# Kernel optimization log

Measured on AMD Instinct MI355X. Metric: run time of the kernel, lower is better.

The kernel has to match this reference:

```python
import jax, jax.numpy as jnp
import numpy as np

N_QUBITS = 12
N_LAYERS = 2
INPUT_DIM = 8
HIDDEN_DIM = 4
SEQ_LEN = 16
BATCH = 64


def _apply_1q(state, gate, wire):
    # state: (B,) + (2,)*n complex64; gate: (2,2) or (B,2,2)
    s = jnp.moveaxis(state, wire + 1, 1)
    sh = s.shape
    s = s.reshape(sh[0], 2, -1)
    if gate.ndim == 2:
        s = jnp.einsum('ij,bjk->bik', gate, s)
    else:
        s = jnp.einsum('bij,bjk->bik', gate, s)
    return jnp.moveaxis(s.reshape(sh), 1, wire + 1)


def _apply_cnot(state, c, t):
    s = jnp.moveaxis(state, (c + 1, t + 1), (1, 2))  # (B,2,2,rest)
    s = jnp.concatenate([s[:, :1], s[:, 1:, ::-1]], axis=1)  # flip target where control=1
    return jnp.moveaxis(s, (1, 2), (c + 1, t + 1))


def _rx_gates(angles):
    # per-sample RX(theta) = [[cos(t/2), -i sin(t/2)], [-i sin(t/2), cos(t/2)]]
    c = jnp.cos(angles / 2).astype(jnp.complex64)
    s = (-1j) * jnp.sin(angles / 2).astype(jnp.complex64)
    return jnp.stack([jnp.stack([c, s], -1), jnp.stack([s, c], -1)], -2)  # (B,2,2)


def _rot_gate(phi, theta, omega):
    # PennyLane Rot(phi,theta,omega) = RZ(omega) RY(theta) RZ(phi)
    c = jnp.cos(theta / 2).astype(jnp.complex64)
    s = jnp.sin(theta / 2).astype(jnp.complex64)
    m00 = jnp.exp(-0.5j * (phi + omega)) * c
    m01 = -jnp.exp(0.5j * (phi - omega)) * s
    m10 = jnp.exp(-0.5j * (phi - omega)) * s
    m11 = jnp.exp(0.5j * (phi + omega)) * c
    return jnp.stack([jnp.stack([m00, m01]), jnp.stack([m10, m11])])


def _circuit(angles, weights):
    # angles: (B, n_qubits); weights: (L, n_qubits, 3) -> (B, n_qubits) PauliZ expvals
    n = N_QUBITS
    B = angles.shape[0]
    state = jnp.zeros((B,) + (2,) * n, jnp.complex64)
    state = state.at[(slice(None),) + (0,) * n].set(1.0)
    for i in range(angles.shape[1]):
        state = _apply_1q(state, _rx_gates(angles[:, i]), i)
    for l in range(N_LAYERS):
        for i in range(n):
            state = _apply_1q(state, _rot_gate(weights[l, i, 0], weights[l, i, 1], weights[l, i, 2]), i)
        r = l % (n - 1) + 1  # StronglyEntanglingLayers default ranges
        for i in range(n):
            state = _apply_cnot(state, i, (i + r) % n)
    p = state.real ** 2 + state.imag ** 2
    z = []
    for i in range(n):
        q = jnp.moveaxis(p, i + 1, 1).reshape(B, 2, -1).sum(-1)
        z.append(q[:, 0] - q[:, 1])
    return jnp.stack(z, axis=1)


def setup_inputs() -> dict:
    key = jax.random.key(0)
    ks = jax.random.split(key, 16)
    inp = {
        'inputs': jax.random.normal(ks[0], (SEQ_LEN, BATCH, INPUT_DIM), jnp.float32),
        'forget_weights': jax.random.normal(ks[1], (N_LAYERS, N_QUBITS, 3), jnp.float32),
        'input_weights': jax.random.normal(ks[2], (N_LAYERS, N_QUBITS, 3), jnp.float32),
        'update_weights': jax.random.normal(ks[3], (N_LAYERS, N_QUBITS, 3), jnp.float32),
        'output_weights': jax.random.normal(ks[4], (N_LAYERS, N_QUBITS, 3), jnp.float32),
        'fW': jax.random.normal(ks[5], (HIDDEN_DIM, N_QUBITS), jnp.float32) * 0.3,
        'fb': jax.random.normal(ks[6], (HIDDEN_DIM,), jnp.float32) * 0.1,
        'iW': jax.random.normal(ks[7], (HIDDEN_DIM, N_QUBITS), jnp.float32) * 0.3,
        'ib': jax.random.normal(ks[8], (HIDDEN_DIM,), jnp.float32) * 0.1,
        'uW': jax.random.normal(ks[9], (HIDDEN_DIM, N_QUBITS), jnp.float32) * 0.3,
        'ub': jax.random.normal(ks[10], (HIDDEN_DIM,), jnp.float32) * 0.1,
        'oW': jax.random.normal(ks[11], (HIDDEN_DIM, N_QUBITS), jnp.float32) * 0.3,
        'ob': jax.random.normal(ks[12], (HIDDEN_DIM,), jnp.float32) * 0.1,
    }
    return inp


def reference(inputs, forget_weights, input_weights, update_weights, output_weights,
              fW, fb, iW, ib, uW, ub, oW, ob):
    S, B, D = inputs.shape
    H = fb.shape[0]
    h0 = jnp.zeros((B, H), inputs.dtype)
    c0 = jnp.zeros((B, H), inputs.dtype)

    def step(carry, x):
        hx, cx = carry
        comb = jnp.concatenate([x, hx], axis=1)  # (B, n_qubits)
        f = jax.nn.sigmoid(_circuit(comb, forget_weights) @ fW.T + fb)
        i = jax.nn.sigmoid(_circuit(comb, input_weights) @ iW.T + ib)
        g = jnp.tanh(_circuit(comb, update_weights) @ uW.T + ub)
        o = jax.nn.sigmoid(_circuit(comb, output_weights) @ oW.T + ob)
        cx = f * cx + i * g
        hx = o * jnp.tanh(cx)
        return (hx, cx), hx

    (hx, cx), outputs = jax.lax.scan(jax.checkpoint(step), (h0, c0), inputs)
    return outputs, hx, cx
```

## Files before the change

### kernel.cpp

```cpp
#include <hip/hip_runtime.h>
#include <math.h>

#define AGENT __HIP_MEMORY_SCOPE_AGENT


__device__ __forceinline__ float ftanh(float x) {
    x = fminf(fmaxf(x, -15.f), 15.f);
    const float e = __expf(2.f * x);
    return (e - 1.f) / (e + 1.f);
}
__device__ __forceinline__ float fsigm(float x) { return 1.f / (1.f + __expf(-x)); }
__device__ __forceinline__ float gld(const float* p) {
    return __hip_atomic_load(p, __ATOMIC_RELAXED, AGENT);
}

#define CMUL(dr, di, xr, xi, yr, yi) \
    do { dr = (xr)*(yr) - (xi)*(yi); di = (xr)*(yi) + (xi)*(yr); } while (0)

template<int CTRL>
__device__ __forceinline__ float dppf(float x) {
    return __int_as_float(__builtin_amdgcn_update_dpp(
        0, __float_as_int(x), CTRL, 0xF, 0xF, true));
}

template<int CTRL>
__device__ __forceinline__ void dpprot(float ar[8], float ai[8],
                                       float por, float poi, float ppr, float ppi) {
#pragma unroll
    for (int j = 0; j < 8; ++j) {
        const float qr = dppf<CTRL>(ar[j]);
        const float qi = dppf<CTRL>(ai[j]);
        const float nr = por*ar[j] - poi*ai[j] + ppr*qr - ppi*qi;
        const float ni = por*ai[j] + poi*ar[j] + ppr*qi + ppi*qr;
        ar[j] = nr; ai[j] = ni;
    }
}

__device__ __forceinline__ void shflrot32(float ar[8], float ai[8],
                                          float por, float poi, float ppr, float ppi) {
#pragma unroll
    for (int j = 0; j < 8; ++j) {
        const float qr = __shfl_xor(ar[j], 32);
        const float qi = __shfl_xor(ai[j], 32);
        const float nr = por*ar[j] - poi*ai[j] + ppr*qr - ppi*qi;
        const float ni = por*ai[j] + poi*ar[j] + ppr*qi + ppi*qr;
        ar[j] = nr; ai[j] = ni;
    }
}

__device__ __forceinline__ void rot3(float ar[8], float ai[8],
                                     const float* __restrict__ g3) {
    float gm[24];
#pragma unroll
    for (int k = 0; k < 6; ++k) ((float4*)gm)[k] = ((const float4*)g3)[k];
#pragma unroll
    for (int k = 0; k < 3; ++k) {
        const float m0=gm[k*8+0], m1=gm[k*8+1], m2=gm[k*8+2], m3=gm[k*8+3];
        const float m4=gm[k*8+4], m5=gm[k*8+5], m6=gm[k*8+6], m7=gm[k*8+7];
        const int vs = 4 >> k;
#pragma unroll
        for (int p = 0; p < 4; ++p) {
            const int lowm = vs - 1;
            const int j0 = ((p & ~lowm) << 1) | (p & lowm);
            const int j1 = j0 | vs;
            const float a0r = ar[j0], a0i = ai[j0];
            const float a1r = ar[j1], a1i = ai[j1];
            ar[j0] = m0*a0r - m1*a0i + m2*a1r - m3*a1i;
            ai[j0] = m0*a0i + m1*a0r + m2*a1i + m3*a1r;
            ar[j1] = m4*a0r - m5*a0i + m6*a1r - m7*a1i;
            ai[j1] = m4*a0i + m5*a0r + m6*a1i + m7*a1r;
        }
    }
}

__global__ __launch_bounds__(512, 2)
void qlstm_fused(const float* __restrict__ inputs,
                 const float* __restrict__ wf, const float* __restrict__ wi,
                 const float* __restrict__ wu, const float* __restrict__ wo,
                 const float* __restrict__ fW, const float* __restrict__ fb,
                 const float* __restrict__ iW, const float* __restrict__ ib,
                 const float* __restrict__ uW, const float* __restrict__ ub,
                 const float* __restrict__ oW, const float* __restrict__ ob,
                 float* __restrict__ gact,
                 unsigned* __restrict__ ctr,
                 float* __restrict__ out)
{
    __shared__ float2 bufA[4096], bufB[4096];
    __shared__ __align__(16) float rotm[192];
    __shared__ __align__(16) float4 wtab[12];
    __shared__ float Wsh[48];
    __shared__ float zred[8][4];

    const int tid = threadIdx.x;
    const int b = blockIdx.x & 63;
    const int g = blockIdx.x >> 6;
    const int l = tid & 63, w = tid >> 6;

    const float* wsel = (g == 0) ? wf : (g == 1) ? wi : (g == 2) ? wu : wo;
    const float* Wsel = (g == 0) ? fW : (g == 1) ? iW : (g == 2) ? uW : oW;
    const float* bsel = (g == 0) ? fb : (g == 1) ? ib : (g == 2) ? ub : ob;

    if (tid < 24) {
        const int k = tid;
        const float phi = wsel[k*3+0], th = wsel[k*3+1], om = wsel[k*3+2];
        float ct, sth; __sincosf(0.5f * th, &sth, &ct);
        float ca, sa;  __sincosf(0.5f * (phi + om), &sa, &ca);
        float cb, sb2; __sincosf(0.5f * (phi - om), &sb2, &cb);
        float* m = rotm + k * 8;
        m[0] =  ca * ct;  m[1] = -sa * ct;
        m[2] = -cb * sth; m[3] = -sb2 * sth;
        m[4] =  cb * sth; m[5] = -sb2 * sth;
        m[6] =  ca * ct;  m[7] =  sa * ct;
    }
    if (tid < 48) Wsh[tid] = Wsel[tid];
    const float bu = (tid < 4) ? bsel[tid] : 0.f;
    __syncthreads();

    const int MSK[12] = {0x555,0xAAA,0x554,0xAA8,0x550,0xAA0,
                         0x540,0xA80,0x500,0xA00,0x155,0x2AA};
    const int qbase = ((l >> 5) << 8) | (w << 5) | (((l >> 3) & 3) << 3) | (l & 7);
    float4 Qv[8];
#pragma unroll
    for (int s = 0; s < 8; ++s) {
        float q0 = 0.f, q1 = 0.f, q2 = 0.f, q3 = 0.f;
        const int idx = qbase | (s << 9);
#pragma unroll
        for (int p = 0; p < 12; ++p) {
            const float sgn = (__popc(idx & MSK[p]) & 1) ? -1.f : 1.f;
            const int m = 11 - p;
            q0 += sgn * Wsh[m];
            q1 += sgn * Wsh[12 + m];
            q2 += sgn * Wsh[24 + m];
            q3 += sgn * Wsh[36 + m];
        }
        Qv[s] = make_float4(q0, q1, q2, q3);
    }

    const int X0 = (tid << 3) ^ (tid << 2);
    int bitq[7];
#pragma unroll
    for (int qq = 0; qq < 7; ++qq) bitq[qq] = (X0 >> (9 - qq)) & 1;
    const int b11 = (tid >> 8) & 1;
    const int b10 = ((tid >> 7) & 1) ^ b11;
    const int lx  = tid & 1;
    const int wbase = (tid << 3) ^ (tid & 15);
    const int rb1 = ((w << 9) | (((l >> 5) & 1) << 8) |
                     (((l >> 3) & 3) << 3) | (l & 7)) ^ ((l >> 3) & 3);
    const int rb2 = ((l << 3) | w) ^ (l & 15);
    const int be8 = l & 1, be7 = (l >> 1) & 1, be3 = (l >> 5) & 1;

    float c_ = 0.f, h_ = 0.f;

    for (int t = 0; t < 16; ++t) {
        if (tid >= 64 && tid < 72) {
            const int q = tid - 64;
            float sn, cs; __sincosf(0.5f * inputs[t*512 + b*8 + q], &sn, &cs);
            const float* m = rotm + q * 8;
            wtab[q] = make_float4(m[0]*cs + m[3]*sn, m[1]*cs - m[2]*sn,
                                  m[4]*cs + m[7]*sn, m[5]*cs - m[6]*sn);
        }
        if (tid < 4) {
            if (t > 0) {
                while (__hip_atomic_load(&ctr[b*16 + (t-1)],
                                         __ATOMIC_RELAXED, AGENT) < 4u)
                    __builtin_amdgcn_s_sleep(2);
                __threadfence();
                const float* ga = gact + ((t-1)&1)*1024 + b*4 + tid;
                const float f_ = gld(ga),       i_ = gld(ga + 256);
                const float u_ = gld(ga + 512), o_ = gld(ga + 768);
                c_ = f_*c_ + i_*u_;
                h_ = o_*ftanh(c_);
                if (g == 0) out[(t-1)*256 + b*4 + tid] = h_;
            }
            float sn, cs; __sincosf(0.5f * h_, &sn, &cs);
            const float* m = rotm + (8 + tid) * 8;
            wtab[8 + tid] = make_float4(m[0]*cs + m[3]*sn, m[1]*cs - m[2]*sn,
                                        m[4]*cs + m[7]*sn, m[5]*cs - m[6]*sn);
        }
        __syncthreads();

        const float* wf4 = (const float*)wtab;
        float Pr, Pi;
        {
            const float2 f0 = *(const float2*)(wf4 + 2*4 + bitq[0]*2);
            Pr = f0.x; Pi = f0.y;
#pragma unroll
            for (int qq = 1; qq < 7; ++qq) {
                const float2 f = *(const float2*)(wf4 + (2+qq)*4 + bitq[qq]*2);
                float nr, ni; CMUL(nr, ni, Pr, Pi, f.x, f.y);
                Pr = nr; Pi = ni;
            }
        }
        const float4 R0 = wtab[0], R1 = wtab[1];
        const float4 R9 = wtab[9], RA = wtab[10], RB = wtab[11];
        const float v0sr = b11 ? R0.z : R0.x, v0si = b11 ? R0.w : R0.y;
        const float v0or = b11 ? R0.x : R0.z, v0oi = b11 ? R0.y : R0.w;
        const float v1sr = b10 ? R1.z : R1.x, v1si = b10 ? R1.w : R1.y;
        const float v1or = b10 ? R1.x : R1.z, v1oi = b10 ? R1.y : R1.w;
        float Er, Ei, Og, Oh;
        CMUL(Er, Ei, v0sr, v0si, v1sr, v1si);
        CMUL(Og, Oh, v0or, v0oi, v1or, v1oi);
        float PEr, PEi, POr, POi;
        CMUL(PEr, PEi, Pr, Pi, Er, Ei);
        CMUL(POr, POi, Pr, Pi, Og, Oh);
        const float w9lr = lx ? R9.z : R9.x, w9li = lx ? R9.w : R9.y;
        const float w9hr = lx ? R9.x : R9.z, w9hi = lx ? R9.y : R9.w;
        float m0r,m0i, m1r,m1i, m2r,m2i, m3r,m3i;
        CMUL(m0r,m0i, w9lr,w9li, RA.x,RA.y);
        CMUL(m1r,m1i, w9lr,w9li, RA.z,RA.w);
        CMUL(m2r,m2i, w9hr,w9hi, RA.x,RA.y);
        CMUL(m3r,m3i, w9hr,w9hi, RA.z,RA.w);
        float ttr[8], tti[8];
        CMUL(ttr[0],tti[0], m0r,m0i, RB.x,RB.y);
        CMUL(ttr[1],tti[1], m0r,m0i, RB.z,RB.w);
        CMUL(ttr[2],tti[2], m1r,m1i, RB.x,RB.y);
        CMUL(ttr[3],tti[3], m1r,m1i, RB.z,RB.w);
        CMUL(ttr[4],tti[4], m2r,m2i, RB.x,RB.y);
        CMUL(ttr[5],tti[5], m2r,m2i, RB.z,RB.w);
        CMUL(ttr[6],tti[6], m3r,m3i, RB.x,RB.y);
        CMUL(ttr[7],tti[7], m3r,m3i, RB.z,RB.w);
        float ar[8], ai[8];
        CMUL(ar[0],ai[0], PEr,PEi, ttr[0],tti[0]);
        CMUL(ar[1],ai[1], POr,POi, ttr[1],tti[1]);
        CMUL(ar[2],ai[2], PEr,PEi, ttr[3],tti[3]);
        CMUL(ar[3],ai[3], POr,POi, ttr[2],tti[2]);
        CMUL(ar[4],ai[4], PEr,PEi, ttr[6],tti[6]);
        CMUL(ar[5],ai[5], POr,POi, ttr[7],tti[7]);
        CMUL(ar[6],ai[6], PEr,PEi, ttr[5],tti[5]);
        CMUL(ar[7],ai[7], POr,POi, ttr[4],tti[4]);

        rot3(ar, ai, rotm + 168);
        {
            const float4 row = *(const float4*)(rotm + 160 + (be8 << 2));
            const float por = be8 ? row.z : row.x, poi = be8 ? row.w : row.y;
            const float ppr = be8 ? row.x : row.z, ppi = be8 ? row.y : row.w;
            dpprot<0xB1>(ar, ai, por, poi, ppr, ppi);
        }
        {
            const float4 row = *(const float4*)(rotm + 152 + (be7 << 2));
            const float por = be7 ? row.z : row.x, poi = be7 ? row.w : row.y;
            const float ppr = be7 ? row.x : row.z, ppi = be7 ? row.y : row.w;
            dpprot<0x4E>(ar, ai, por, poi, ppr, ppi);
        }
        {
            const float4 row = *(const float4*)(rotm + 120 + (be3 << 2));
            const float por = be3 ? row.z : row.x, poi = be3 ? row.w : row.y;
            const float ppr = be3 ? row.x : row.z, ppi = be3 ? row.y : row.w;
            shflrot32(ar, ai, por, poi, ppr, ppi);
        }
#pragma unroll
        for (int s = 0; s < 8; ++s)
            bufA[wbase ^ s] = make_float2(ar[s], ai[s]);
        __syncthreads();
#pragma unroll
        for (int s = 0; s < 8; ++s) {
            const float2 v = bufA[(rb1 | (s << 5)) ^ ((s & 3) << 2)];
            ar[s] = v.x; ai[s] = v.y;
        }
        rot3(ar, ai, rotm + 128);
#pragma unroll
        for (int s = 0; s < 8; ++s)
            bufB[wbase ^ s] = make_float2(ar[s], ai[s]);
        __syncthreads();
#pragma unroll
        for (int s = 0; s < 8; ++s) {
            const float2 v = bufB[rb2 | (s << 9)];
            ar[s] = v.x; ai[s] = v.y;
        }
        rot3(ar, ai, rotm + 96);

        float a0 = 0.f, a1 = 0.f, a2 = 0.f, a3 = 0.f;
#pragma unroll
        for (int s = 0; s < 8; ++s) {
            const float p = ar[s]*ar[s] + ai[s]*ai[s];
            a0 += p * Qv[s].x; a1 += p * Qv[s].y;
            a2 += p * Qv[s].z; a3 += p * Qv[s].w;
        }
#pragma unroll
        for (int off = 32; off > 0; off >>= 1) {
            a0 += __shfl_down(a0, off);
            a1 += __shfl_down(a1, off);
            a2 += __shfl_down(a2, off);
            a3 += __shfl_down(a3, off);
        }
        if (l == 0) {
            zred[w][0] = a0; zred[w][1] = a1; zred[w][2] = a2; zred[w][3] = a3;
        }
        __syncthreads();
        if (tid < 4) {
            float tot = bu;
#pragma unroll
            for (int wv = 0; wv < 8; ++wv) tot += zred[wv][tid];
            const float act = (g == 2) ? ftanh(tot) : fsigm(tot);
            __hip_atomic_store(&gact[(t&1)*1024 + g*256 + b*4 + tid], act,
                               __ATOMIC_RELAXED, AGENT);
        }
        if (tid == 0)
            __hip_atomic_fetch_add(&ctr[b*16 + t], 1u, __ATOMIC_RELEASE, AGENT);
    }

    if (g == 0 && tid < 4) {
        while (__hip_atomic_load(&ctr[b*16 + 15], __ATOMIC_RELAXED, AGENT) < 4u)
            __builtin_amdgcn_s_sleep(2);
        __threadfence();
        const float* ga = gact + 1024 + b*4 + tid;
        const float f_ = gld(ga),       i_ = gld(ga + 256);
        const float u_ = gld(ga + 512), o_ = gld(ga + 768);
        const float cn = f_*c_ + i_*u_;
        const float hn = o_*ftanh(cn);
        out[3840 + b*4 + tid] = hn;
        out[4096 + b*4 + tid] = hn;
        out[4352 + b*4 + tid] = cn;
    }
}

extern "C" void kernel_launch(void* const* d_in, const int* in_sizes, int n_in,
                              void* d_out, int out_size, void* d_ws, size_t ws_size,
                              hipStream_t stream) {
    (void)in_sizes; (void)n_in; (void)out_size; (void)ws_size;
    const float* inputs = (const float*)d_in[0];
    const float* wf = (const float*)d_in[1];
    const float* wi = (const float*)d_in[2];
    const float* wu = (const float*)d_in[3];
    const float* wo = (const float*)d_in[4];
    const float* fW = (const float*)d_in[5];
    const float* fb = (const float*)d_in[6];
    const float* iW = (const float*)d_in[7];
    const float* ib = (const float*)d_in[8];
    const float* uW = (const float*)d_in[9];
    const float* ub = (const float*)d_in[10];
    const float* oW = (const float*)d_in[11];
    const float* ob = (const float*)d_in[12];
    float* out = (float*)d_out;
    unsigned* ctr = (unsigned*)d_ws;
    float* gact = (float*)d_ws + 1024;

    hipMemsetAsync(ctr, 0, 1024 * sizeof(unsigned), stream);

    void* args[] = { (void*)&inputs, (void*)&wf, (void*)&wi, (void*)&wu, (void*)&wo,
                     (void*)&fW, (void*)&fb, (void*)&iW, (void*)&ib,
                     (void*)&uW, (void*)&ub, (void*)&oW, (void*)&ob,
                     (void*)&gact, (void*)&ctr, (void*)&out };
    hipError_t err = hipLaunchCooperativeKernel((const void*)qlstm_fused,
                                                dim3(256), dim3(512),
                                                args, 0, stream);
    if (err != hipSuccess) {
        qlstm_fused<<<dim3(256), dim3(512), 0, stream>>>(
            inputs, wf, wi, wu, wo, fW, fb, iW, ib, uW, ub, oW, ob,
            gact, ctr, out);
    }
}
```

Before: 168.2 us.

## Prefetch input-angle gates, hoist rotation matrices to registers, cheaper reduction

Double-buffers the input-encoding gate table so step t+1's sincos is computed during step t. The input-only product of the first nine qubit factors is now computed before the cross-block spin-wait and barrier, leaving only the hidden-state-dependent part on the critical path. The rotation matrices and per-lane DPP/shuffle coefficients are loaded once into registers instead of being reloaded from LDS every step. The four-value wave reduction is also replaced by a butterfly that folds the accumulators into one lane-distributed value, cutting shuffle count. The cost is higher register pressure from 72+ extra live floats, which risks spills under the 512x2 launch bound.

Measured after the change: 204.0 us (median of 3 runs). +21.3%, slower.

```diff
diff --git a/kernel.cpp b/kernel.cpp
--- a/kernel.cpp
+++ b/kernel.cpp
@@ -48,11 +48,8 @@
     }
 }
 
-__device__ __forceinline__ void rot3(float ar[8], float ai[8],
-                                     const float* __restrict__ g3) {
-    float gm[24];
-#pragma unroll
-    for (int k = 0; k < 6; ++k) ((float4*)gm)[k] = ((const float4*)g3)[k];
+__device__ __forceinline__ void rot3r(float ar[8], float ai[8],
+                                      const float* gm) {
 #pragma unroll
     for (int k = 0; k < 3; ++k) {
         const float m0=gm[k*8+0], m1=gm[k*8+1], m2=gm[k*8+2], m3=gm[k*8+3];
@@ -87,7 +84,8 @@
 {
     __shared__ float2 bufA[4096], bufB[4096];
     __shared__ __align__(16) float rotm[192];
-    __shared__ __align__(16) float4 wtab[12];
+    __shared__ __align__(16) float4 wtabx[2][8];
+    __shared__ __align__(16) float4 wtabh[4];
     __shared__ float Wsh[48];
     __shared__ float zred[8][4];
 
@@ -116,6 +114,32 @@
     const float bu = (tid < 4) ? bsel[tid] : 0.f;
     __syncthreads();
 
+    if (tid >= 64 && tid < 72) {
+        const int q = tid - 64;
+        float sn, cs; __sincosf(0.5f * inputs[b*8 + q], &sn, &cs);
+        const float* m = rotm + q * 8;
+        wtabx[0][q] = make_float4(m[0]*cs + m[3]*sn, m[1]*cs - m[2]*sn,
+                                  m[4]*cs + m[7]*sn, m[5]*cs - m[6]*sn);
+    }
+
+    const int be8 = l & 1, be7 = (l >> 1) & 1, be3 = (l >> 5) & 1;
+    float rT[24], rM[24], rL[24];
+#pragma unroll
+    for (int k = 0; k < 6; ++k) {
+        ((float4*)rT)[k] = ((const float4*)(rotm + 168))[k];
+        ((float4*)rM)[k] = ((const float4*)(rotm + 128))[k];
+        ((float4*)rL)[k] = ((const float4*)(rotm +  96))[k];
+    }
+    const float4 r8v = *(const float4*)(rotm + 160 + (be8 << 2));
+    const float por8 = be8 ? r8v.z : r8v.x, poi8 = be8 ? r8v.w : r8v.y;
+    const float ppr8 = be8 ? r8v.x : r8v.z, ppi8 = be8 ? r8v.y : r8v.w;
+    const float4 r7v = *(const float4*)(rotm + 152 + (be7 << 2));
+    const float por7 = be7 ? r7v.z : r7v.x, poi7 = be7 ? r7v.w : r7v.y;
+    const float ppr7 = be7 ? r7v.x : r7v.z, ppi7 = be7 ? r7v.y : r7v.w;
+    const float4 r3v = *(const float4*)(rotm + 120 + (be3 << 2));
+    const float por3 = be3 ? r3v.z : r3v.x, poi3 = be3 ? r3v.w : r3v.y;
+    const float ppr3 = be3 ? r3v.x : r3v.z, ppi3 = be3 ? r3v.y : r3v.w;
+
     const int MSK[12] = {0x555,0xAAA,0x554,0xAA8,0x550,0xAA0,
                          0x540,0xA80,0x500,0xA00,0x155,0x2AA};
     const int qbase = ((l >> 5) << 8) | (w << 5) | (((l >> 3) & 3) << 3) | (l & 7);
@@ -147,18 +171,45 @@
     const int rb1 = ((w << 9) | (((l >> 5) & 1) << 8) |
                      (((l >> 3) & 3) << 3) | (l & 7)) ^ ((l >> 3) & 3);
     const int rb2 = ((l << 3) | w) ^ (l & 15);
-    const int be8 = l & 1, be7 = (l >> 1) & 1, be3 = (l >> 5) & 1;
 
     float c_ = 0.f, h_ = 0.f;
 
+    __syncthreads();
+
     for (int t = 0; t < 16; ++t) {
-        if (tid >= 64 && tid < 72) {
+        const int cur = t & 1;
+        if (t < 15 && tid >= 64 && tid < 72) {
             const int q = tid - 64;
-            float sn, cs; __sincosf(0.5f * inputs[t*512 + b*8 + q], &sn, &cs);
+            float sn, cs; __sincosf(0.5f * inputs[(t+1)*512 + b*8 + q], &sn, &cs);
             const float* m = rotm + q * 8;
-            wtab[q] = make_float4(m[0]*cs + m[3]*sn, m[1]*cs - m[2]*sn,
-                                  m[4]*cs + m[7]*sn, m[5]*cs - m[6]*sn);
-        }
+            wtabx[cur ^ 1][q] = make_float4(m[0]*cs + m[3]*sn, m[1]*cs - m[2]*sn,
+                                            m[4]*cs + m[7]*sn, m[5]*cs - m[6]*sn);
+        }
+
+        const float* wx = (const float*)&wtabx[cur][0];
+        const float2 f2 = *(const float2*)(wx +  8 + bitq[0]*2);
+        const float2 f3 = *(const float2*)(wx + 12 + bitq[1]*2);
+        const float2 f4 = *(const float2*)(wx + 16 + bitq[2]*2);
+        const float2 f5 = *(const float2*)(wx + 20 + bitq[3]*2);
+        const float2 f6 = *(const float2*)(wx + 24 + bitq[4]*2);
+        const float2 f7 = *(const float2*)(wx + 28 + bitq[5]*2);
+        float a23r,a23i, a45r,a45i, a67r,a67i, p47r,p47i, P6r,P6i;
+        CMUL(a23r,a23i, f2.x,f2.y, f3.x,f3.y);
+        CMUL(a45r,a45i, f4.x,f4.y, f5.x,f5.y);
+        CMUL(a67r,a67i, f6.x,f6.y, f7.x,f7.y);
+        CMUL(p47r,p47i, a45r,a45i, a67r,a67i);
+        CMUL(P6r,P6i,   a23r,a23i, p47r,p47i);
+        const float4 R0 = wtabx[cur][0], R1 = wtabx[cur][1];
+        const float v0sr = b11 ? R0.z : R0.x, v0si = b11 ? R0.w : R0.y;
+        const float v0or = b11 ? R0.x : R0.z, v0oi = b11 ? R0.y : R0.w;
+        const float v1sr = b10 ? R1.z : R1.x, v1si = b10 ? R1.w : R1.y;
+        const float v1or = b10 ? R1.x : R1.z, v1oi = b10 ? R1.y : R1.w;
+        float Er,Ei, Og,Oh, PEr,PEi, POr,POi;
+        CMUL(Er,Ei, v0sr,v0si, v1sr,v1si);
+        CMUL(Og,Oh, v0or,v0oi, v1or,v1oi);
+        CMUL(PEr,PEi, P6r,P6i, Er,Ei);
+        CMUL(POr,POi, P6r,P6i, Og,Oh);
+
         if (tid < 4) {
             if (t > 0) {
                 while (__hip_atomic_load(&ctr[b*16 + (t-1)],
@@ -174,35 +225,16 @@
             }
             float sn, cs; __sincosf(0.5f * h_, &sn, &cs);
             const float* m = rotm + (8 + tid) * 8;
-            wtab[8 + tid] = make_float4(m[0]*cs + m[3]*sn, m[1]*cs - m[2]*sn,
-                                        m[4]*cs + m[7]*sn, m[5]*cs - m[6]*sn);
+            wtabh[tid] = make_float4(m[0]*cs + m[3]*sn, m[1]*cs - m[2]*sn,
+                                     m[4]*cs + m[7]*sn, m[5]*cs - m[6]*sn);
         }
         __syncthreads();
 
-        const float* wf4 = (const float*)wtab;
-        float Pr, Pi;
-        {
-            const float2 f0 = *(const float2*)(wf4 + 2*4 + bitq[0]*2);
-            Pr = f0.x; Pi = f0.y;
-#pragma unroll
-            for (int qq = 1; qq < 7; ++qq) {
-                const float2 f = *(const float2*)(wf4 + (2+qq)*4 + bitq[qq]*2);
-                float nr, ni; CMUL(nr, ni, Pr, Pi, f.x, f.y);
-                Pr = nr; Pi = ni;
-            }
-        }
-        const float4 R0 = wtab[0], R1 = wtab[1];
-        const float4 R9 = wtab[9], RA = wtab[10], RB = wtab[11];
-        const float v0sr = b11 ? R0.z : R0.x, v0si = b11 ? R0.w : R0.y;
-        const float v0or = b11 ? R0.x : R0.z, v0oi = b11 ? R0.y : R0.w;
-        const float v1sr = b10 ? R1.z : R1.x, v1si = b10 ? R1.w : R1.y;
-        const float v1or = b10 ? R1.x : R1.z, v1oi = b10 ? R1.y : R1.w;
-        float Er, Ei, Og, Oh;
-        CMUL(Er, Ei, v0sr, v0si, v1sr, v1si);
-        CMUL(Og, Oh, v0or, v0oi, v1or, v1oi);
-        float PEr, PEi, POr, POi;
-        CMUL(PEr, PEi, Pr, Pi, Er, Ei);
-        CMUL(POr, POi, Pr, Pi, Og, Oh);
+        const float4 W8 = wtabh[0], R9 = wtabh[1], RA = wtabh[2], RB = wtabh[3];
+        const float w8r = bitq[6] ? W8.z : W8.x, w8i = bitq[6] ? W8.w : W8.y;
+        float FEr,FEi, FOr,FOi;
+        CMUL(FEr,FEi, PEr,PEi, w8r,w8i);
+        CMUL(FOr,FOi, POr,POi, w8r,w8i);
         const float w9lr = lx ? R9.z : R9.x, w9li = lx ? R9.w : R9.y;
         const float w9hr = lx ? R9.x : R9.z, w9hi = lx ? R9.y : R9.w;
         float m0r,m0i, m1r,m1i, m2r,m2i, m3r,m3i;
@@ -220,34 +252,20 @@
         CMUL(ttr[6],tti[6], m3r,m3i, RB.x,RB.y);
         CMUL(ttr[7],tti[7], m3r,m3i, RB.z,RB.w);
         float ar[8], ai[8];
-        CMUL(ar[0],ai[0], PEr,PEi, ttr[0],tti[0]);
-        CMUL(ar[1],ai[1], POr,POi, ttr[1],tti[1]);
-        CMUL(ar[2],ai[2], PEr,PEi, ttr[3],tti[3]);
-        CMUL(ar[3],ai[3], POr,POi, ttr[2],tti[2]);
-        CMUL(ar[4],ai[4], PEr,PEi, ttr[6],tti[6]);
-        CMUL(ar[5],ai[5], POr,POi, ttr[7],tti[7]);
-        CMUL(ar[6],ai[6], PEr,PEi, ttr[5],tti[5]);
-        CMUL(ar[7],ai[7], POr,POi, ttr[4],tti[4]);
-
-        rot3(ar, ai, rotm + 168);
-        {
-            const float4 row = *(const float4*)(rotm + 160 + (be8 << 2));
-            const float por = be8 ? row.z : row.x, poi = be8 ? row.w : row.y;
-            const float ppr = be8 ? row.x : row.z, ppi = be8 ? row.y : row.w;
-            dpprot<0xB1>(ar, ai, por, poi, ppr, ppi);
-        }
-        {
-            const float4 row = *(const float4*)(rotm + 152 + (be7 << 2));
-            const float por = be7 ? row.z : row.x, poi = be7 ? row.w : row.y;
-            const float ppr = be7 ? row.x : row.z, ppi = be7 ? row.y : row.w;
-            dpprot<0x4E>(ar, ai, por, poi, ppr, ppi);
-        }
-        {
-            const float4 row = *(const float4*)(rotm + 120 + (be3 << 2));
-            const float por = be3 ? row.z : row.x, poi = be3 ? row.w : row.y;
-            const float ppr = be3 ? row.x : row.z, ppi = be3 ? row.y : row.w;
-            shflrot32(ar, ai, por, poi, ppr, ppi);
-        }
+        CMUL(ar[0],ai[0], FEr,FEi, ttr[0],tti[0]);
+        CMUL(ar[1],ai[1], FOr,FOi, ttr[1],tti[1]);
+        CMUL(ar[2],ai[2], FEr,FEi, ttr[3],tti[3]);
+        CMUL(ar[3],ai[3], FOr,FOi, ttr[2],tti[2]);
+        CMUL(ar[4],ai[4], FEr,FEi, ttr[6],tti[6]);
+        CMUL(ar[5],ai[5], FOr,FOi, ttr[7],tti[7]);
+        CMUL(ar[6],ai[6], FEr,FEi, ttr[5],tti[5]);
+        CMUL(ar[7],ai[7], FOr,FOi, ttr[4],tti[4]);
+
+        rot3r(ar, ai, rT);
+        dpprot<0xB1>(ar, ai, por8, poi8, ppr8, ppi8);
+        dpprot<0x4E>(ar, ai, por7, poi7, ppr7, ppi7);
+        shflrot32(ar, ai, por3, poi3, ppr3, ppi3);
+
 #pragma unroll
         for (int s = 0; s < 8; ++s)
             bufA[wbase ^ s] = make_float2(ar[s], ai[s]);
@@ -257,7 +275,7 @@
             const float2 v = bufA[(rb1 | (s << 5)) ^ ((s & 3) << 2)];
             ar[s] = v.x; ai[s] = v.y;
         }
-        rot3(ar, ai, rotm + 128);
+        rot3r(ar, ai, rM);
 #pragma unroll
         for (int s = 0; s < 8; ++s)
             bufB[wbase ^ s] = make_float2(ar[s], ai[s]);
@@ -267,7 +285,7 @@
             const float2 v = bufB[rb2 | (s << 9)];
             ar[s] = v.x; ai[s] = v.y;
         }
-        rot3(ar, ai, rotm + 96);
+        rot3r(ar, ai, rL);
 
         float a0 = 0.f, a1 = 0.f, a2 = 0.f, a3 = 0.f;
 #pragma unroll
@@ -276,17 +294,24 @@
             a0 += p * Qv[s].x; a1 += p * Qv[s].y;
             a2 += p * Qv[s].z; a3 += p * Qv[s].w;
         }
-#pragma unroll
-        for (int off = 32; off > 0; off >>= 1) {
-            a0 += __shfl_down(a0, off);
-            a1 += __shfl_down(a1, off);
-            a2 += __shfl_down(a2, off);
-            a3 += __shfl_down(a3, off);
-        }
-        if (l == 0) {
-            zred[w][0] = a0; zred[w][1] = a1; zred[w][2] = a2; zred[w][3] = a3;
+        {
+            const float s1 = (l & 1) ? a0 : a1;
+            const float k1 = (l & 1) ? a1 : a0;
+            const float r01 = k1 + __shfl_xor(s1, 1);
+            const float s2 = (l & 1) ? a2 : a3;
+            const float k2 = (l & 1) ? a3 : a2;
+            const float r23 = k2 + __shfl_xor(s2, 1);
+            const float s3 = (l & 2) ? r01 : r23;
+            const float k3 = (l & 2) ? r23 : r01;
+            float rc = k3 + __shfl_xor(s3, 2);
+            rc += __shfl_xor(rc, 4);
+            rc += __shfl_xor(rc, 8);
+            rc += __shfl_xor(rc, 16);
+            rc += __shfl_xor(rc, 32);
+            if (l < 4) zred[w][l] = rc;
         }
         __syncthreads();
+
         if (tid < 4) {
             float tot = bu;
 #pragma unroll
```
